# Kernel optimization log

Hardware: AMD Instinct MI355X
Metric: run time of the kernel (lower is better)

## Reference

```python
import jax, jax.numpy as jnp
import numpy as np

KERNEL = 3          # route_nms_kernel
MAX_ROUTES = 256    # max_routes (topk per image)
STRIDE = 4.0        # route_stride
MIN_SIZE = 32.0     # route_min_size
MAX_SIZE = 512.0    # route_max_size
POWER = 2.0         # route_score_power
B, H, W = 32, 512, 512


def setup_inputs() -> dict:
    key = jax.random.key(0)
    k1, k2, k3 = jax.random.split(key, 3)
    return {
        "route_logits": jax.random.normal(k1, (B, 1, H, W), dtype=jnp.float32),
        "scale_logits": jax.random.normal(k2, (B, 1, H, W), dtype=jnp.float32),
        "uncertainty_logits": jax.random.normal(k3, (B, 1, H, W), dtype=jnp.float32),
        "image_h": 2048,
        "image_w": 2048,
    }


def _local_max_pool(x):
    # x: [H, W]; 3x3 max pool, stride 1, pad kernel//2 (torch F.max_pool2d pads with -inf)
    pad = KERNEL // 2
    return jax.lax.reduce_window(x, -jnp.inf, jax.lax.max,
                                 (KERNEL, KERNEL), (1, 1),
                                 [(pad, pad), (pad, pad)])


def reference(route_logits, scale_logits, uncertainty_logits, image_h, image_w):
    # score_map = sigmoid(logits)^power * (1 - 0.35*sigmoid(uncertainty))  (use_route_uncertainty=True)
    score_map = jnp.power(jax.nn.sigmoid(route_logits), POWER)
    score_map = score_map * (1.0 - 0.35 * jax.nn.sigmoid(uncertainty_logits))
    img_h = jnp.float32(image_h)
    img_w = jnp.float32(image_w)
    width = route_logits.shape[-1]

    def per_image(batch_idx, scores2d, scale2d, unc2d):
        pooled = _local_max_pool(scores2d)
        filtered = jnp.where(scores2d == pooled, scores2d, -1.0)  # masked_fill(~mask, -1)
        values, indices = jax.lax.top_k(filtered.reshape(-1), MAX_ROUTES)
        valid = values > 0.0  # torch filters values>0; here kept as fixed-shape mask
        ys = indices // width
        xs = indices % width
        cx = (xs.astype(jnp.float32) + 0.5) * STRIDE
        cy = (ys.astype(jnp.float32) + 0.5) * STRIDE
        scale_g = scale2d[ys, xs]
        unc = jax.nn.sigmoid(unc2d[ys, xs])
        side = MIN_SIZE + jax.nn.sigmoid(scale_g) * (MAX_SIZE - MIN_SIZE)
        side = side * (1.0 + 0.25 * unc)
        half = side * 0.5
        x1 = jnp.clip(cx - half, 0.0, img_w - 1.0)
        y1 = jnp.clip(cy - half, 0.0, img_h - 1.0)
        x2 = jnp.clip(cx + half, 1.0, img_w)
        y2 = jnp.clip(cy + half, 1.0, img_h)
        rois = jnp.stack([jnp.full_like(x1, batch_idx), x1, y1, x2, y2], axis=1)  # [K,5]
        rois = jnp.where(valid[:, None], rois, 0.0)
        vals = jnp.where(valid, values, 0.0)
        return rois, vals, valid

    batch_ids = jnp.arange(route_logits.shape[0], dtype=jnp.float32)
    rois, scores, valid = jax.vmap(per_image)(
        batch_ids, score_map[:, 0], scale_logits[:, 0], uncertainty_logits[:, 0])
    # rois: [B, K, 5], scores: [B, K], valid: [B, K] (per_image_counts = valid.sum(-1))
    return rois, scores, valid
```

## Files before the change

kernel.cpp:

```cpp
#include <hip/hip_runtime.h>
#include <cstdint>
#include <cstddef>

#define BATCH 32
#define IMH 512
#define IMW 512
#define KMAX 256

#define RPW 4
#define NBLKX 2
#define NYG (IMH / RPW)
#define NL1 (NBLKX * NYG)
#define NM1 (NL1 / 4)
#define NMID (NM1 / 4)
#define WCAP 256

#define TPB2 512

typedef unsigned long long u64;

__device__ __forceinline__ float sigmoidf_(float x) {
    return 1.0f / (1.0f + expf(-x));
}
__device__ __forceinline__ float scoref_(float r, float u) {
    const float sg = sigmoidf_(r);
    return sg * sg * (1.0f - 0.35f * sigmoidf_(u));
}

#define SHF(v, jj, dm) do {                                         \
    const u64 o_ = __shfl_xor((v), (jj), 64);                       \
    const bool take_ = ((((lane & (jj)) == 0) == (dm)) == ((v) < o_)); \
    (v) = take_ ? o_ : (v);                                         \
} while (0)

#define RMAX(a, b) do {                                             \
    const u64 hi_ = ((a) > (b)) ? (a) : (b);                        \
    const u64 lo_ = ((a) > (b)) ? (b) : (a);                        \
    (a) = hi_; (b) = lo_;                                           \
} while (0)

#define RMIN(a, b) do {                                             \
    const u64 hi_ = ((a) > (b)) ? (a) : (b);                        \
    const u64 lo_ = ((a) > (b)) ? (b) : (a);                        \
    (a) = lo_; (b) = hi_;                                           \
} while (0)

__device__ __forceinline__ void clean256(u64& v0, u64& v1, u64& v2, u64& v3,
                                         const int lane) {
    RMAX(v0, v2); RMAX(v1, v3);
    RMAX(v0, v1); RMAX(v2, v3);
    #pragma unroll
    for (int j = 32; j > 0; j >>= 1) {
        SHF(v0, j, true); SHF(v1, j, true); SHF(v2, j, true); SHF(v3, j, true);
    }
}

__device__ __forceinline__ void sort256(u64& v0, u64& v1, u64& v2, u64& v3,
                                        const int lane) {
    #pragma unroll
    for (int k = 2; k <= 32; k <<= 1) {
        #pragma unroll
        for (int j = k >> 1; j > 0; j >>= 1) {
            const bool dm = ((lane & k) == 0);
            SHF(v0, j, dm); SHF(v1, j, dm); SHF(v2, j, dm); SHF(v3, j, dm);
        }
    }
    #pragma unroll
    for (int j = 32; j > 0; j >>= 1) {
        SHF(v0, j, true); SHF(v1, j, false); SHF(v2, j, true); SHF(v3, j, false);
    }
    RMAX(v0, v1); RMIN(v2, v3);
    #pragma unroll
    for (int j = 32; j > 0; j >>= 1) {
        SHF(v0, j, true); SHF(v1, j, true); SHF(v2, j, false); SHF(v3, j, false);
    }
    clean256(v0, v1, v2, v3, lane);
}

__device__ __forceinline__ void sort128(u64& v0, u64& v1, const int lane) {
    #pragma unroll
    for (int k = 2; k <= 32; k <<= 1) {
        #pragma unroll
        for (int j = k >> 1; j > 0; j >>= 1) {
            const bool dm = ((lane & k) == 0);
            SHF(v0, j, dm); SHF(v1, j, dm);
        }
    }
    #pragma unroll
    for (int j = 32; j > 0; j >>= 1) {
        SHF(v0, j, true); SHF(v1, j, false);
    }
    RMAX(v0, v1);
    #pragma unroll
    for (int j = 32; j > 0; j >>= 1) {
        SHF(v0, j, true); SHF(v1, j, true);
    }
}

__device__ __forceinline__ void merge256(u64& v0, u64& v1, u64& v2, u64& v3,
                                         u64 w0, u64 w1, u64 w2, u64 w3,
                                         const int lane) {
    const int rl = 63 ^ lane;
    const u64 b0 = __shfl(w3, rl, 64);
    const u64 b1 = __shfl(w2, rl, 64);
    const u64 b2 = __shfl(w1, rl, 64);
    const u64 b3 = __shfl(w0, rl, 64);
    v0 = (v0 > b0) ? v0 : b0;
    v1 = (v1 > b1) ? v1 : b1;
    v2 = (v2 > b2) ? v2 : b2;
    v3 = (v3 > b3) ? v3 : b3;
    clean256(v0, v1, v2, v3, lane);
}

__global__ __launch_bounds__(128)
void score_nms_kernel(const float* __restrict__ route,
                      const float* __restrict__ unc,
                      u64* __restrict__ top) {
    const int b    = blockIdx.z;
    const int w    = threadIdx.x >> 6;
    const int lane = threadIdx.x & 63;
    const int yg   = blockIdx.y * 2 + w;
    const int y0   = yg * RPW;
    const int x0   = blockIdx.x * 256 + lane * 4;
    const int list = yg * NBLKX + blockIdx.x;

    __shared__ u64 lcand[2 * WCAP];
    u64* myR = lcand + w * WCAP;

    const float* rB = route + (size_t)b * IMH * IMW;
    const float* uB = unc   + (size_t)b * IMH * IMW;

    int ex = -1;
    if (lane == 0)       ex = x0 - 1;
    else if (lane == 63) ex = x0 + 4;
    const bool eAct = (ex >= 0 && ex < IMW);

    const u64 laneMaskLt = (1ull << lane) - 1ull;
    int wcnt = 0;

    float sP[4], hP1[4], hP2[4];
    #pragma unroll
    for (int j = 0; j < 4; ++j) { sP[j] = -INFINITY; hP1[j] = -INFINITY; hP2[j] = -INFINITY; }

    const int ylast = y0 + RPW;
    bool v = (y0 - 1 >= 0);
    float4 r4, u4; float er = 0.f, eu = 0.f;
    if (v) {
        r4 = *(const float4*)(rB + (size_t)(y0 - 1) * IMW + x0);
        u4 = *(const float4*)(uB + (size_t)(y0 - 1) * IMW + x0);
        if (eAct) { er = rB[(size_t)(y0 - 1) * IMW + ex]; eu = uB[(size_t)(y0 - 1) * IMW + ex]; }
    }

    for (int y = y0 - 1; y <= ylast; ++y) {
        const int yn = y + 1;
        const bool vn = (yn <= ylast) && (yn < IMH);
        float4 r4n, u4n; float ern = 0.f, eun = 0.f;
        if (vn) {
            r4n = *(const float4*)(rB + (size_t)yn * IMW + x0);
            u4n = *(const float4*)(uB + (size_t)yn * IMW + x0);
            if (eAct) { ern = rB[(size_t)yn * IMW + ex]; eun = uB[(size_t)yn * IMW + ex]; }
        }

        float sC[4], hmC[4];
        float es = -INFINITY;
        if (v && eAct) es = scoref_(er, eu);
        if (v) {
            sC[0] = scoref_(r4.x, u4.x);
            sC[1] = scoref_(r4.y, u4.y);
            sC[2] = scoref_(r4.z, u4.z);
            sC[3] = scoref_(r4.w, u4.w);
        } else {
            sC[0] = sC[1] = sC[2] = sC[3] = -INFINITY;
        }
        float lft = __shfl_up(sC[3], 1, 64);
        if (lane == 0) lft = es;
        float rgt = __shfl_down(sC[0], 1, 64);
        if (lane == 63) rgt = es;
        if (v) {
            hmC[0] = fmaxf(fmaxf(lft,   sC[0]), sC[1]);
            hmC[1] = fmaxf(fmaxf(sC[0], sC[1]), sC[2]);
            hmC[2] = fmaxf(fmaxf(sC[1], sC[2]), sC[3]);
            hmC[3] = fmaxf(fmaxf(sC[2], sC[3]), rgt);
        } else {
            hmC[0] = hmC[1] = hmC[2] = hmC[3] = -INFINITY;
        }

        if (y >= y0 + 1) {
            const int yo = y - 1;
            bool p[4]; int cntT = 0;
            #pragma unroll
            for (int j = 0; j < 4; ++j) {
                const float m9 = fmaxf(fmaxf(hP2[j], hP1[j]), hmC[j]);
                p[j] = (sP[j] >= m9);
                cntT += p[j] ? 1 : 0;
            }
            const u64 B0 = __ballot(cntT & 1);
            const u64 B1 = __ballot(cntT & 2);
            const u64 B2 = __ballot(cntT & 4);
            const int total = __popcll(B0) + 2 * __popcll(B1) + 4 * __popcll(B2);
            if (total > 0) {
                const int prefix = __popcll(B0 & laneMaskLt) + 2 * __popcll(B1 & laneMaskLt)
                                 + 4 * __popcll(B2 & laneMaskLt);
                int mb = wcnt + prefix;
                #pragma unroll
                for (int j = 0; j < 4; ++j) {
                    if (p[j]) {
                        const unsigned idx = (unsigned)(yo * IMW + (x0 + j));
                        const u64 key = ((u64)__float_as_uint(sP[j]) << 32) | (unsigned)(~idx);
                        if (mb < WCAP) myR[mb] = key;
                        ++mb;
                    }
                }
                wcnt += total;
            }
        }

        #pragma unroll
        for (int j = 0; j < 4; ++j) { hP2[j] = hP1[j]; hP1[j] = hmC[j]; sP[j] = sC[j]; }
        r4 = r4n; u4 = u4n; er = ern; eu = eun; v = vn;
    }

    const int m = (wcnt < WCAP) ? wcnt : WCAP;
    u64 a0, a1, a2, a3;
    if (m <= 128) {
        a0 = (lane      < m) ? myR[lane]      : 0ull;
        a1 = (lane + 64 < m) ? myR[lane + 64] : 0ull;
        sort128(a0, a1, lane);
        a2 = 0ull; a3 = 0ull;
    } else {
        a0 = (lane       < m) ? myR[lane]       : 0ull;
        a1 = (lane + 64  < m) ? myR[lane + 64]  : 0ull;
        a2 = (lane + 128 < m) ? myR[lane + 128] : 0ull;
        a3 = (lane + 192 < m) ? myR[lane + 192] : 0ull;
        sort256(a0, a1, a2, a3, lane);
    }

    u64* seg = top + ((size_t)b * NL1 + list) * KMAX;
    seg[lane]       = a0;
    seg[lane + 64]  = a1;
    seg[lane + 128] = a2;
    seg[lane + 192] = a3;
}

__global__ __launch_bounds__(128)
void merge4_kernel(const u64* __restrict__ in, int nin,
                   u64* __restrict__ out_) {
    const int w    = threadIdx.x >> 6;
    const int lane = threadIdx.x & 63;
    const int o    = blockIdx.x * 2 + w;
    const int b    = blockIdx.y;
    const int nout = nin / 4;
    if (o >= nout) return;

    const u64* L = in + ((size_t)b * nin + o * 4) * KMAX;

    u64 a0 = L[lane],            a1 = L[lane + 64],
        a2 = L[lane + 128],      a3 = L[lane + 192];
    {
        const u64 w0 = L[KMAX + lane],       w1 = L[KMAX + lane + 64],
                  w2 = L[KMAX + lane + 128], w3 = L[KMAX + lane + 192];
        merge256(a0, a1, a2, a3, w0, w1, w2, w3, lane);
    }
    u64 c0 = L[2 * KMAX + lane],        c1 = L[2 * KMAX + lane + 64],
        c2 = L[2 * KMAX + lane + 128],  c3 = L[2 * KMAX + lane + 192];
    {
        const u64 w0 = L[3 * KMAX + lane],       w1 = L[3 * KMAX + lane + 64],
                  w2 = L[3 * KMAX + lane + 128], w3 = L[3 * KMAX + lane + 192];
        merge256(c0, c1, c2, c3, w0, w1, w2, w3, lane);
    }
    merge256(a0, a1, a2, a3, c0, c1, c2, c3, lane);

    u64* out = out_ + ((size_t)b * nout + o) * KMAX;
    out[lane]       = a0;
    out[lane + 64]  = a1;
    out[lane + 128] = a2;
    out[lane + 192] = a3;
}

__global__ __launch_bounds__(TPB2)
void tail_kernel(const u64* __restrict__ mid,
                 const float* __restrict__ scale,
                 const float* __restrict__ unc,
                 const int* __restrict__ imh,
                 const int* __restrict__ imw,
                 float* __restrict__ rois,
                 float* __restrict__ scoresOut,
                 float* __restrict__ validOut) {
    const int b   = blockIdx.x;
    const int tid = threadIdx.x;

    __shared__ u64 bufA[NMID * KMAX];
    __shared__ u64 bufB[(NMID / 2) * KMAX];

    const u64* tb = mid + (size_t)b * NMID * KMAX;
    for (int i = tid; i < NMID * KMAX; i += TPB2) bufA[i] = tb[i];
    __syncthreads();

    u64* src = bufA;
    u64* dst = bufB;
    int nl = NMID;
    while (nl > 1) {
        const int half = nl >> 1;
        const int E = half * KMAX;
        for (int p = tid; p < E; p += TPB2) {
            const int h = p >> 8;
            const int i = p & (KMAX - 1);
            const u64 a = src[(2 * h) * KMAX + i];
            const u64 c = src[(2 * h + 1) * KMAX + (KMAX - 1 - i)];
            dst[p] = (a > c) ? a : c;
        }
        __syncthreads();
        for (int j = KMAX >> 1; j > 0; j >>= 1) {
            for (int p = tid; p < (E >> 1); p += TPB2) {
                const int i   = ((p & ~(j - 1)) << 1) | (p & (j - 1));
                const int ixj = i | j;
                const u64 a = dst[i];
                const u64 c = dst[ixj];
                if (a < c) { dst[i] = c; dst[ixj] = a; }
            }
            __syncthreads();
        }
        u64* t = src; src = dst; dst = t;
        nl = half;
    }

    if (tid < KMAX) {
        const u64 k = src[tid];
        const float value = __uint_as_float((unsigned)(k >> 32));
        const bool valid  = (k != 0ull) && (value > 0.0f);

        float r0 = 0.f, r1 = 0.f, r2 = 0.f, r3 = 0.f, r4 = 0.f, sv = 0.f, vv = 0.f;
        if (valid) {
            const unsigned idx = ~(unsigned)(k & 0xFFFFFFFFull);
            const int y = (int)(idx / IMW);
            const int x = (int)(idx % IMW);
            const float cx = ((float)x + 0.5f) * 4.0f;
            const float cy = ((float)y + 0.5f) * 4.0f;
            const float sg = scale[(size_t)b * IMH * IMW + idx];
            const float uu = unc[(size_t)b * IMH * IMW + idx];
            const float su = sigmoidf_(uu);
            float side = 32.0f + sigmoidf_(sg) * (512.0f - 32.0f);
            side = side * (1.0f + 0.25f * su);
            const float half2 = side * 0.5f;
            const float fw = (float)imw[0];
            const float fh = (float)imh[0];
            r0 = (float)b;
            r1 = fminf(fmaxf(cx - half2, 0.0f), fw - 1.0f);
            r2 = fminf(fmaxf(cy - half2, 0.0f), fh - 1.0f);
            r3 = fminf(fmaxf(cx + half2, 1.0f), fw);
            r4 = fminf(fmaxf(cy + half2, 1.0f), fh);
            sv = value;
            vv = 1.0f;
        }
        float* roiP = rois + ((size_t)b * KMAX + tid) * 5;
        roiP[0] = r0; roiP[1] = r1; roiP[2] = r2; roiP[3] = r3; roiP[4] = r4;
        scoresOut[b * KMAX + tid] = sv;
        validOut[b * KMAX + tid]  = vv;
    }
}

extern "C" void kernel_launch(void* const* d_in, const int* in_sizes, int n_in,
                              void* d_out, int out_size, void* d_ws, size_t ws_size,
                              hipStream_t stream) {
    const float* route = (const float*)d_in[0];
    const float* scale = (const float*)d_in[1];
    const float* unc   = (const float*)d_in[2];
    const int*   imh   = (const int*)d_in[3];
    const int*   imw   = (const int*)d_in[4];

    u64* top  = (u64*)d_ws;
    u64* mid1 = top  + (size_t)BATCH * NL1 * KMAX;
    u64* mid2 = mid1 + (size_t)BATCH * NM1 * KMAX;

    float* rois      = (float*)d_out;
    float* scoresOut = rois + (size_t)BATCH * KMAX * 5;
    float* validOut  = scoresOut + (size_t)BATCH * KMAX;

    dim3 grid1(NBLKX, NYG / 2, BATCH);
    score_nms_kernel<<<grid1, 128, 0, stream>>>(route, unc, top);

    dim3 grid2(NM1 / 2, BATCH);
    merge4_kernel<<<grid2, 128, 0, stream>>>(top, NL1, mid1);

    dim3 grid3(NMID / 2, BATCH);
    merge4_kernel<<<grid3, 128, 0, stream>>>(mid1, NM1, mid2);

    tail_kernel<<<BATCH, TPB2, 0, stream>>>(mid2, scale, unc,
                                            imh, imw, rois, scoresOut, validOut);
}
```

Before: 60.74 us.

## Fuse merge stages and tail into one per-image wavefront-merge kernel

Replaces the two merge4 launches and the shared-memory bitonic tail kernel with a single 1024-thread block per image. Each wave merges 8 sorted lists straight from global memory using register shuffles, then further wave-level merge rounds run in LDS, and wave 0 emits the ROIs. This removes two kernel launches and the intermediate global round-trips, and swaps the barrier-heavy LDS bitonic sort for shuffle merges. The trade-off is that only 32 blocks run the whole reduction, so parallelism in the merge phase is much lower.

```diff
diff --git a/kernel.cpp b/kernel.cpp
--- a/kernel.cpp
+++ b/kernel.cpp
@@ -11,11 +11,7 @@
 #define NBLKX 2
 #define NYG (IMH / RPW)
 #define NL1 (NBLKX * NYG)
-#define NM1 (NL1 / 4)
-#define NMID (NM1 / 4)
 #define WCAP 256
-
-#define TPB2 512
 
 typedef unsigned long long u64;
 
@@ -110,6 +106,29 @@
     v2 = (v2 > b2) ? v2 : b2;
     v3 = (v3 > b3) ? v3 : b3;
     clean256(v0, v1, v2, v3, lane);
+}
+
+__device__ __forceinline__ void load256(const u64* p, u64& v0, u64& v1,
+                                        u64& v2, u64& v3, const int lane) {
+    v0 = p[lane]; v1 = p[lane + 64]; v2 = p[lane + 128]; v3 = p[lane + 192];
+}
+__device__ __forceinline__ void store256(u64* p, u64 v0, u64 v1,
+                                         u64 v2, u64 v3, const int lane) {
+    p[lane] = v0; p[lane + 64] = v1; p[lane + 128] = v2; p[lane + 192] = v3;
+}
+
+__device__ __forceinline__ void merge4s(const u64* p, size_t st,
+                                        u64& a0, u64& a1, u64& a2, u64& a3,
+                                        const int lane) {
+    load256(p, a0, a1, a2, a3, lane);
+    u64 w0, w1, w2, w3;
+    load256(p + st, w0, w1, w2, w3, lane);
+    merge256(a0, a1, a2, a3, w0, w1, w2, w3, lane);
+    u64 c0, c1, c2, c3;
+    load256(p + 2 * st, c0, c1, c2, c3, lane);
+    load256(p + 3 * st, w0, w1, w2, w3, lane);
+    merge256(c0, c1, c2, c3, w0, w1, w2, w3, lane);
+    merge256(a0, a1, a2, a3, c0, c1, c2, c3, lane);
 }
 
 __global__ __launch_bounds__(128)
@@ -236,126 +255,98 @@
     }
 
     u64* seg = top + ((size_t)b * NL1 + list) * KMAX;
-    seg[lane]       = a0;
-    seg[lane + 64]  = a1;
-    seg[lane + 128] = a2;
-    seg[lane + 192] = a3;
-}
-
-__global__ __launch_bounds__(128)
-void merge4_kernel(const u64* __restrict__ in, int nin,
-                   u64* __restrict__ out_) {
+    store256(seg, a0, a1, a2, a3, lane);
+}
+
+__global__ __launch_bounds__(1024)
+void fused_tail_kernel(const u64* __restrict__ top,
+                       const float* __restrict__ scale,
+                       const float* __restrict__ unc,
+                       const int* __restrict__ imh,
+                       const int* __restrict__ imw,
+                       float* __restrict__ rois,
+                       float* __restrict__ scoresOut,
+                       float* __restrict__ validOut) {
+    const int b    = blockIdx.x;
     const int w    = threadIdx.x >> 6;
     const int lane = threadIdx.x & 63;
-    const int o    = blockIdx.x * 2 + w;
-    const int b    = blockIdx.y;
-    const int nout = nin / 4;
-    if (o >= nout) return;
-
-    const u64* L = in + ((size_t)b * nin + o * 4) * KMAX;
-
-    u64 a0 = L[lane],            a1 = L[lane + 64],
-        a2 = L[lane + 128],      a3 = L[lane + 192];
-    {
-        const u64 w0 = L[KMAX + lane],       w1 = L[KMAX + lane + 64],
-                  w2 = L[KMAX + lane + 128], w3 = L[KMAX + lane + 192];
+
+    __shared__ u64 L[32 * KMAX];
+
+    const u64* tb = top + (size_t)b * NL1 * KMAX;
+
+    #pragma unroll
+    for (int i = 0; i < 2; ++i) {
+        const int o = 2 * w + i;
+        const u64* G = tb + (size_t)o * 8 * KMAX;
+        u64 a0, a1, a2, a3, c0, c1, c2, c3;
+        merge4s(G,             KMAX, a0, a1, a2, a3, lane);
+        merge4s(G + 4 * KMAX,  KMAX, c0, c1, c2, c3, lane);
+        merge256(a0, a1, a2, a3, c0, c1, c2, c3, lane);
+        store256(L + (size_t)o * KMAX, a0, a1, a2, a3, lane);
+    }
+    __syncthreads();
+
+    if (w < 8) {
+        u64 a0, a1, a2, a3;
+        merge4s(L + (size_t)(4 * w) * KMAX, KMAX, a0, a1, a2, a3, lane);
+        store256(L + (size_t)(4 * w) * KMAX, a0, a1, a2, a3, lane);
+    }
+    __syncthreads();
+
+    if (w < 2) {
+        u64 a0, a1, a2, a3;
+        merge4s(L + (size_t)(16 * w) * KMAX, (size_t)4 * KMAX, a0, a1, a2, a3, lane);
+        store256(L + (size_t)(16 * w) * KMAX, a0, a1, a2, a3, lane);
+    }
+    __syncthreads();
+
+    if (w == 0) {
+        u64 a0, a1, a2, a3, w0, w1, w2, w3;
+        load256(L, a0, a1, a2, a3, lane);
+        load256(L + (size_t)16 * KMAX, w0, w1, w2, w3, lane);
         merge256(a0, a1, a2, a3, w0, w1, w2, w3, lane);
-    }
-    u64 c0 = L[2 * KMAX + lane],        c1 = L[2 * KMAX + lane + 64],
-        c2 = L[2 * KMAX + lane + 128],  c3 = L[2 * KMAX + lane + 192];
-    {
-        const u64 w0 = L[3 * KMAX + lane],       w1 = L[3 * KMAX + lane + 64],
-                  w2 = L[3 * KMAX + lane + 128], w3 = L[3 * KMAX + lane + 192];
-        merge256(c0, c1, c2, c3, w0, w1, w2, w3, lane);
-    }
-    merge256(a0, a1, a2, a3, c0, c1, c2, c3, lane);
-
-    u64* out = out_ + ((size_t)b * nout + o) * KMAX;
-    out[lane]       = a0;
-    out[lane + 64]  = a1;
-    out[lane + 128] = a2;
-    out[lane + 192] = a3;
-}
-
-__global__ __launch_bounds__(TPB2)
-void tail_kernel(const u64* __restrict__ mid,
-                 const float* __restrict__ scale,
-                 const float* __restrict__ unc,
-                 const int* __restrict__ imh,
-                 const int* __restrict__ imw,
-                 float* __restrict__ rois,
-                 float* __restrict__ scoresOut,
-                 float* __restrict__ validOut) {
-    const int b   = blockIdx.x;
-    const int tid = threadIdx.x;
-
-    __shared__ u64 bufA[NMID * KMAX];
-    __shared__ u64 bufB[(NMID / 2) * KMAX];
-
-    const u64* tb = mid + (size_t)b * NMID * KMAX;
-    for (int i = tid; i < NMID * KMAX; i += TPB2) bufA[i] = tb[i];
-    __syncthreads();
-
-    u64* src = bufA;
-    u64* dst = bufB;
-    int nl = NMID;
-    while (nl > 1) {
-        const int half = nl >> 1;
-        const int E = half * KMAX;
-        for (int p = tid; p < E; p += TPB2) {
-            const int h = p >> 8;
-            const int i = p & (KMAX - 1);
-            const u64 a = src[(2 * h) * KMAX + i];
-            const u64 c = src[(2 * h + 1) * KMAX + (KMAX - 1 - i)];
-            dst[p] = (a > c) ? a : c;
-        }
-        __syncthreads();
-        for (int j = KMAX >> 1; j > 0; j >>= 1) {
-            for (int p = tid; p < (E >> 1); p += TPB2) {
-                const int i   = ((p & ~(j - 1)) << 1) | (p & (j - 1));
-                const int ixj = i | j;
-                const u64 a = dst[i];
-                const u64 c = dst[ixj];
-                if (a < c) { dst[i] = c; dst[ixj] = a; }
+
+        const float fw = (float)imw[0];
+        const float fh = (float)imh[0];
+        const float* scB = scale + (size_t)b * IMH * IMW;
+        const float* unB = unc   + (size_t)b * IMH * IMW;
+
+        u64 regs[1];
+        (void)regs;
+        #pragma unroll
+        for (int r = 0; r < 4; ++r) {
+            const u64 k = (r == 0) ? a0 : (r == 1) ? a1 : (r == 2) ? a2 : a3;
+            const int slot = r * 64 + lane;
+            const float value = __uint_as_float((unsigned)(k >> 32));
+            const bool valid  = (k != 0ull) && (value > 0.0f);
+
+            float r0 = 0.f, r1 = 0.f, r2 = 0.f, r3 = 0.f, r4 = 0.f, sv = 0.f, vv = 0.f;
+            if (valid) {
+                const unsigned idx = ~(unsigned)(k & 0xFFFFFFFFull);
+                const int y = (int)(idx / IMW);
+                const int x = (int)(idx % IMW);
+                const float cx = ((float)x + 0.5f) * 4.0f;
+                const float cy = ((float)y + 0.5f) * 4.0f;
+                const float sg = scB[idx];
+                const float uu = unB[idx];
+                const float su = sigmoidf_(uu);
+                float side = 32.0f + sigmoidf_(sg) * (512.0f - 32.0f);
+                side = side * (1.0f + 0.25f * su);
+                const float half2 = side * 0.5f;
+                r0 = (float)b;
+                r1 = fminf(fmaxf(cx - half2, 0.0f), fw - 1.0f);
+                r2 = fminf(fmaxf(cy - half2, 0.0f), fh - 1.0f);
+                r3 = fminf(fmaxf(cx + half2, 1.0f), fw);
+                r4 = fminf(fmaxf(cy + half2, 1.0f), fh);
+                sv = value;
+                vv = 1.0f;
             }
-            __syncthreads();
-        }
-        u64* t = src; src = dst; dst = t;
-        nl = half;
-    }
-
-    if (tid < KMAX) {
-        const u64 k = src[tid];
-        const float value = __uint_as_float((unsigned)(k >> 32));
-        const bool valid  = (k != 0ull) && (value > 0.0f);
-
-        float r0 = 0.f, r1 = 0.f, r2 = 0.f, r3 = 0.f, r4 = 0.f, sv = 0.f, vv = 0.f;
-        if (valid) {
-            const unsigned idx = ~(unsigned)(k & 0xFFFFFFFFull);
-            const int y = (int)(idx / IMW);
-            const int x = (int)(idx % IMW);
-            const float cx = ((float)x + 0.5f) * 4.0f;
-            const float cy = ((float)y + 0.5f) * 4.0f;
-            const float sg = scale[(size_t)b * IMH * IMW + idx];
-            const float uu = unc[(size_t)b * IMH * IMW + idx];
-            const float su = sigmoidf_(uu);
-            float side = 32.0f + sigmoidf_(sg) * (512.0f - 32.0f);
-            side = side * (1.0f + 0.25f * su);
-            const float half2 = side * 0.5f;
-            const float fw = (float)imw[0];
-            const float fh = (float)imh[0];
-            r0 = (float)b;
-            r1 = fminf(fmaxf(cx - half2, 0.0f), fw - 1.0f);
-            r2 = fminf(fmaxf(cy - half2, 0.0f), fh - 1.0f);
-            r3 = fminf(fmaxf(cx + half2, 1.0f), fw);
-            r4 = fminf(fmaxf(cy + half2, 1.0f), fh);
-            sv = value;
-            vv = 1.0f;
-        }
-        float* roiP = rois + ((size_t)b * KMAX + tid) * 5;
-        roiP[0] = r0; roiP[1] = r1; roiP[2] = r2; roiP[3] = r3; roiP[4] = r4;
-        scoresOut[b * KMAX + tid] = sv;
-        validOut[b * KMAX + tid]  = vv;
+            float* roiP = rois + ((size_t)b * KMAX + slot) * 5;
+            roiP[0] = r0; roiP[1] = r1; roiP[2] = r2; roiP[3] = r3; roiP[4] = r4;
+            scoresOut[b * KMAX + slot] = sv;
+            validOut[b * KMAX + slot]  = vv;
+        }
     }
 }
 
@@ -368,9 +359,7 @@
     const int*   imh   = (const int*)d_in[3];
     const int*   imw   = (const int*)d_in[4];
 
-    u64* top  = (u64*)d_ws;
-    u64* mid1 = top  + (size_t)BATCH * NL1 * KMAX;
-    u64* mid2 = mid1 + (size_t)BATCH * NM1 * KMAX;
+    u64* top = (u64*)d_ws;
 
     float* rois      = (float*)d_out;
     float* scoresOut = rois + (size_t)BATCH * KMAX * 5;
@@ -379,12 +368,6 @@
     dim3 grid1(NBLKX, NYG / 2, BATCH);
     score_nms_kernel<<<grid1, 128, 0, stream>>>(route, unc, top);
 
-    dim3 grid2(NM1 / 2, BATCH);
-    merge4_kernel<<<grid2, 128, 0, stream>>>(top, NL1, mid1);
-
-    dim3 grid3(NMID / 2, BATCH);
-    merge4_kernel<<<grid3, 128, 0, stream>>>(mid1, NM1, mid2);
-
-    tail_kernel<<<BATCH, TPB2, 0, stream>>>(mid2, scale, unc,
-                                            imh, imw, rois, scoresOut, validOut);
-}
+    fused_tail_kernel<<<BATCH, 1024, 0, stream>>>(top, scale, unc, imh, imw,
+                                                  rois, scoresOut, validOut);
+}
```

New measurement: 86.46 us. +42.4%, slower.

## Fuse second merge4 stage into tail kernel with 1024-thread blocks

Applied to the files above, without the earlier changes.

Removes the second merge4 kernel launch. The tail kernel now runs 16 wavefronts per image; each wavefront merges 4 sorted lists from mid1 in registers and writes the result to shared memory before the existing shared-memory bitonic merge tree. This saves one launch and one global round trip of intermediate lists. In exchange, each tail block does more serial work, and with only 32 blocks the parallelism is lower.

```diff
diff --git a/kernel.cpp b/kernel.cpp
--- a/kernel.cpp
+++ b/kernel.cpp
@@ -12,10 +12,7 @@
 #define NYG (IMH / RPW)
 #define NL1 (NBLKX * NYG)
 #define NM1 (NL1 / 4)
-#define NMID (NM1 / 4)
 #define WCAP 256
-
-#define TPB2 512
 
 typedef unsigned long long u64;
 
@@ -110,6 +107,29 @@
     v2 = (v2 > b2) ? v2 : b2;
     v3 = (v3 > b3) ? v3 : b3;
     clean256(v0, v1, v2, v3, lane);
+}
+
+__device__ __forceinline__ void load256(const u64* p, u64& v0, u64& v1,
+                                        u64& v2, u64& v3, const int lane) {
+    v0 = p[lane]; v1 = p[lane + 64]; v2 = p[lane + 128]; v3 = p[lane + 192];
+}
+__device__ __forceinline__ void store256(u64* p, u64 v0, u64 v1,
+                                         u64 v2, u64 v3, const int lane) {
+    p[lane] = v0; p[lane + 64] = v1; p[lane + 128] = v2; p[lane + 192] = v3;
+}
+
+__device__ __forceinline__ void merge4s(const u64* p,
+                                        u64& a0, u64& a1, u64& a2, u64& a3,
+                                        const int lane) {
+    load256(p, a0, a1, a2, a3, lane);
+    u64 w0, w1, w2, w3;
+    load256(p + KMAX, w0, w1, w2, w3, lane);
+    merge256(a0, a1, a2, a3, w0, w1, w2, w3, lane);
+    u64 c0, c1, c2, c3;
+    load256(p + 2 * KMAX, c0, c1, c2, c3, lane);
+    load256(p + 3 * KMAX, w0, w1, w2, w3, lane);
+    merge256(c0, c1, c2, c3, w0, w1, w2, w3, lane);
+    merge256(a0, a1, a2, a3, c0, c1, c2, c3, lane);
 }
 
 __global__ __launch_bounds__(128)
@@ -236,10 +256,7 @@
     }
 
     u64* seg = top + ((size_t)b * NL1 + list) * KMAX;
-    seg[lane]       = a0;
-    seg[lane + 64]  = a1;
-    seg[lane + 128] = a2;
-    seg[lane + 192] = a3;
+    store256(seg, a0, a1, a2, a3, lane);
 }
 
 __global__ __launch_bounds__(128)
@@ -253,56 +270,45 @@
     if (o >= nout) return;
 
     const u64* L = in + ((size_t)b * nin + o * 4) * KMAX;
-
-    u64 a0 = L[lane],            a1 = L[lane + 64],
-        a2 = L[lane + 128],      a3 = L[lane + 192];
+    u64 a0, a1, a2, a3;
+    merge4s(L, a0, a1, a2, a3, lane);
+
+    u64* out = out_ + ((size_t)b * nout + o) * KMAX;
+    store256(out, a0, a1, a2, a3, lane);
+}
+
+__global__ __launch_bounds__(1024)
+void fused_tail_kernel(const u64* __restrict__ mid,
+                       const float* __restrict__ scale,
+                       const float* __restrict__ unc,
+                       const int* __restrict__ imh,
+                       const int* __restrict__ imw,
+                       float* __restrict__ rois,
+                       float* __restrict__ scoresOut,
+                       float* __restrict__ validOut) {
+    const int b    = blockIdx.x;
+    const int tid  = threadIdx.x;
+    const int w    = tid >> 6;
+    const int lane = tid & 63;
+
+    __shared__ u64 bufA[16 * KMAX];
+    __shared__ u64 bufB[8 * KMAX];
+
     {
-        const u64 w0 = L[KMAX + lane],       w1 = L[KMAX + lane + 64],
-                  w2 = L[KMAX + lane + 128], w3 = L[KMAX + lane + 192];
-        merge256(a0, a1, a2, a3, w0, w1, w2, w3, lane);
-    }
-    u64 c0 = L[2 * KMAX + lane],        c1 = L[2 * KMAX + lane + 64],
-        c2 = L[2 * KMAX + lane + 128],  c3 = L[2 * KMAX + lane + 192];
-    {
-        const u64 w0 = L[3 * KMAX + lane],       w1 = L[3 * KMAX + lane + 64],
-                  w2 = L[3 * KMAX + lane + 128], w3 = L[3 * KMAX + lane + 192];
-        merge256(c0, c1, c2, c3, w0, w1, w2, w3, lane);
-    }
-    merge256(a0, a1, a2, a3, c0, c1, c2, c3, lane);
-
-    u64* out = out_ + ((size_t)b * nout + o) * KMAX;
-    out[lane]       = a0;
-    out[lane + 64]  = a1;
-    out[lane + 128] = a2;
-    out[lane + 192] = a3;
-}
-
-__global__ __launch_bounds__(TPB2)
-void tail_kernel(const u64* __restrict__ mid,
-                 const float* __restrict__ scale,
-                 const float* __restrict__ unc,
-                 const int* __restrict__ imh,
-                 const int* __restrict__ imw,
-                 float* __restrict__ rois,
-                 float* __restrict__ scoresOut,
-                 float* __restrict__ validOut) {
-    const int b   = blockIdx.x;
-    const int tid = threadIdx.x;
-
-    __shared__ u64 bufA[NMID * KMAX];
-    __shared__ u64 bufB[(NMID / 2) * KMAX];
-
-    const u64* tb = mid + (size_t)b * NMID * KMAX;
-    for (int i = tid; i < NMID * KMAX; i += TPB2) bufA[i] = tb[i];
+        const u64* G = mid + ((size_t)b * NM1 + 4 * w) * KMAX;
+        u64 a0, a1, a2, a3;
+        merge4s(G, a0, a1, a2, a3, lane);
+        store256(bufA + (size_t)w * KMAX, a0, a1, a2, a3, lane);
+    }
     __syncthreads();
 
     u64* src = bufA;
     u64* dst = bufB;
-    int nl = NMID;
+    int nl = 16;
     while (nl > 1) {
         const int half = nl >> 1;
         const int E = half * KMAX;
-        for (int p = tid; p < E; p += TPB2) {
+        for (int p = tid; p < E; p += 1024) {
             const int h = p >> 8;
             const int i = p & (KMAX - 1);
             const u64 a = src[(2 * h) * KMAX + i];
@@ -311,7 +317,7 @@
         }
         __syncthreads();
         for (int j = KMAX >> 1; j > 0; j >>= 1) {
-            for (int p = tid; p < (E >> 1); p += TPB2) {
+            for (int p = tid; p < (E >> 1); p += 1024) {
                 const int i   = ((p & ~(j - 1)) << 1) | (p & (j - 1));
                 const int ixj = i | j;
                 const u64 a = dst[i];
@@ -369,8 +375,7 @@
     const int*   imw   = (const int*)d_in[4];
 
     u64* top  = (u64*)d_ws;
-    u64* mid1 = top  + (size_t)BATCH * NL1 * KMAX;
-    u64* mid2 = mid1 + (size_t)BATCH * NM1 * KMAX;
+    u64* mid1 = top + (size_t)BATCH * NL1 * KMAX;
 
     float* rois      = (float*)d_out;
     float* scoresOut = rois + (size_t)BATCH * KMAX * 5;
@@ -382,9 +387,6 @@
     dim3 grid2(NM1 / 2, BATCH);
     merge4_kernel<<<grid2, 128, 0, stream>>>(top, NL1, mid1);
 
-    dim3 grid3(NMID / 2, BATCH);
-    merge4_kernel<<<grid3, 128, 0, stream>>>(mid1, NM1, mid2);
-
-    tail_kernel<<<BATCH, TPB2, 0, stream>>>(mid2, scale, unc,
-                                            imh, imw, rois, scoresOut, validOut);
-}
+    fused_tail_kernel<<<BATCH, 1024, 0, stream>>>(mid1, scale, unc, imh, imw,
+                                                  rois, scoresOut, validOut);
+}
```

New measurement: 62.72 us. 3.3% more time.
